# Optimization experiments

Hardware: AMD Instinct MI355X
Metric: run time of the kernel (lower is better)

The kernel has to match this reference:

```python
import jax, jax.numpy as jnp
import numpy as np

N_HEADS = 32
N_KV = 8
HEAD_DIM = 64
DIM = 2048
B, T = 4, 1024


def apply_rope(x, cos, sin):
    # x: [B, H, T, D]; cos/sin: [T, D//2]
    Tlen = x.shape[2]
    c = cos[:Tlen][None, None]  # [1,1,T,D/2]
    s = sin[:Tlen][None, None]
    x_even = x[..., 0::2]
    x_odd = x[..., 1::2]
    r_even = x_even * c - x_odd * s
    r_odd = x_even * s + x_odd * c
    # interleave back: out[...,0::2]=r_even, out[...,1::2]=r_odd
    return jnp.stack([r_even, r_odd], axis=-1).reshape(x.shape)


def setup_inputs() -> dict:
    key = jax.random.key(0)
    ks = jax.random.split(key, 7)
    sc = 0.02
    return {
        "x": jax.random.normal(ks[0], (B, T, DIM), jnp.float32),
        "cos": jax.random.normal(ks[1], (T, HEAD_DIM // 2), jnp.float32),
        "sin": jax.random.normal(ks[2], (T, HEAD_DIM // 2), jnp.float32),
        "Wq": jax.random.normal(ks[3], (N_HEADS * HEAD_DIM, DIM), jnp.float32) * sc,
        "Wk": jax.random.normal(ks[4], (N_KV * HEAD_DIM, DIM), jnp.float32) * sc,
        "Wv": jax.random.normal(ks[5], (N_KV * HEAD_DIM, DIM), jnp.float32) * sc,
        "Wo": jax.random.normal(ks[6], (DIM, N_HEADS * HEAD_DIM), jnp.float32) * sc,
    }


def reference(x, cos, sin, Wq, Wk, Wv, Wo):
    Bb, Tt, _ = x.shape
    rep = N_HEADS // N_KV
    # projections (torch Linear: y = x @ W.T)
    q = (x @ Wq.T).reshape(Bb, Tt, N_HEADS, HEAD_DIM).transpose(0, 2, 1, 3)
    k = (x @ Wk.T).reshape(Bb, Tt, N_KV, HEAD_DIM).transpose(0, 2, 1, 3)
    v = (x @ Wv.T).reshape(Bb, Tt, N_KV, HEAD_DIM).transpose(0, 2, 1, 3)
    q = apply_rope(q, cos, sin)
    k = apply_rope(k, cos, sin)
    k = jnp.repeat(k, rep, axis=1)  # [B, n_heads, T, D]
    v = jnp.repeat(v, rep, axis=1)
    scale = HEAD_DIM ** (-0.5)
    scores = jnp.einsum('bhqd,bhkd->bhqk', q, k) * scale
    causal = jnp.triu(jnp.ones((Tt, Tt), dtype=bool), k=1)
    scores = jnp.where(causal[None, None], -jnp.inf, scores)
    attn = jax.nn.softmax(scores, axis=-1)
    out = jnp.einsum('bhqk,bhkd->bhqd', attn, v)
    out = out.transpose(0, 2, 1, 3).reshape(Bb, Tt, N_HEADS * HEAD_DIM)
    return out @ Wo.T
```

## Files before the change

kernel.cpp:

```cpp
#include <hip/hip_runtime.h>
#include <math.h>

#define GAS __attribute__((address_space(1)))
#define LAS __attribute__((address_space(3)))

typedef __attribute__((ext_vector_type(4))) float f32x4;
typedef __attribute__((ext_vector_type(8))) short bf16x8;

#define MFMA(a,b,c) __builtin_amdgcn_mfma_f32_16x16x32_bf16((a),(b),(c),0,0,0)

__device__ __forceinline__ void gl_lds16(const void* g, void* l) {
    __builtin_amdgcn_global_load_lds((const GAS unsigned*)g, (LAS unsigned*)l, 16, 0, 0);
}

__device__ __forceinline__ short f2bf(float f) {
    union { float f; unsigned u; } v; v.f = f;
    unsigned r = (v.u + 0x7fff + ((v.u >> 16) & 1)) >> 16;
    return (short)r;
}

__device__ __forceinline__ void castN(const float* __restrict__ s, short* __restrict__ d,
                                      int n4, int gid, int gsz) {
    for (int i = gid; i < n4; i += gsz) {
        float4 v = ((const float4*)s)[i];
        short4 o = make_short4(f2bf(v.x), f2bf(v.y), f2bf(v.z), f2bf(v.w));
        ((short4*)d)[i] = o;
    }
}

__global__ __launch_bounds__(256)
void cast_all(const float* __restrict__ x,  const float* __restrict__ wq,
              const float* __restrict__ wk, const float* __restrict__ wv,
              const float* __restrict__ wo,
              short* __restrict__ xb, short* __restrict__ wqkv, short* __restrict__ wob) {
    int gid = blockIdx.x*256 + threadIdx.x;
    int gsz = gridDim.x*256;
    castN(x,  xb,               (4096*2048)/4, gid, gsz);
    castN(wq, wqkv,             (2048*2048)/4, gid, gsz);
    castN(wk, wqkv + 2048*2048, (512*2048)/4,  gid, gsz);
    castN(wv, wqkv + 2560*2048, (512*2048)/4,  gid, gsz);
    castN(wo, wob,              (2048*2048)/4, gid, gsz);
}

template<int MODE>
__global__ __launch_bounds__(256)
void gemm_mfma(const short* __restrict__ A, const short* __restrict__ Bw,
               int M, int N, int K, float* __restrict__ Cf,
               short* __restrict__ qo, short* __restrict__ ko, short* __restrict__ vo,
               const float* __restrict__ cosb, const float* __restrict__ sinb)
{
    __shared__ short As[128*32];
    __shared__ short Bs[128*32];
    const int tid = threadIdx.x;
    const int lane = tid & 63, wv = tid >> 6;
    const int wm = wv >> 1, wn = wv & 1;
    const int m0 = blockIdx.y*128, n0 = blockIdx.x*128;
    const int l15 = lane & 15, quad = lane >> 4;

    f32x4 acc[4][4] = {};

    const int srow = lane >> 2, skc = (lane & 3)*8;
    const short* gA0 = A  + (size_t)(m0 + wv*32 + srow)*K + skc;
    const short* gB0 = Bw + (size_t)(n0 + wv*32 + srow)*K + skc;
    short* lA = As + wv*1024;
    short* lB = Bs + wv*1024;

    for (int k0 = 0; k0 < K; k0 += 32) {
        __syncthreads();
        gl_lds16(gA0 + k0,        lA);
        gl_lds16(gA0 + 16*K + k0, lA + 512);
        gl_lds16(gB0 + k0,        lB);
        gl_lds16(gB0 + 16*K + k0, lB + 512);
        __syncthreads();
        bf16x8 af[4], bfr[4];
        #pragma unroll
        for (int t = 0; t < 4; t++) {
            af[t]  = *(const bf16x8*)&As[(wm*64 + t*16 + l15)*32 + quad*8];
            bfr[t] = *(const bf16x8*)&Bs[(wn*64 + t*16 + l15)*32 + quad*8];
        }
        #pragma unroll
        for (int i = 0; i < 4; i++)
            #pragma unroll
            for (int j = 0; j < 4; j++)
                acc[i][j] = MFMA(af[i], bfr[j], acc[i][j]);
    }

    if (MODE == 0) {
        #pragma unroll
        for (int i = 0; i < 4; i++)
            #pragma unroll
            for (int j = 0; j < 4; j++) {
                int n  = n0 + wn*64 + j*16 + l15;
                int mb = m0 + wm*64 + i*16 + quad*4;
                #pragma unroll
                for (int r = 0; r < 4; r++)
                    Cf[(size_t)(mb + r)*N + n] = acc[i][j][r];
            }
    } else {
        #pragma unroll
        for (int i = 0; i < 4; i++)
            #pragma unroll
            for (int j = 0; j < 4; j++) {
                int n  = n0 + wn*64 + j*16 + l15;
                int mb = m0 + wm*64 + i*16 + quad*4;
                if (n >= 2560) {
                    int bq = mb >> 10, t0 = mb & 1023;
                    int hv = (n - 2560) >> 6, d = (n - 2560) & 63;
                    short4 s4 = make_short4(f2bf(acc[i][j][0]), f2bf(acc[i][j][1]),
                                            f2bf(acc[i][j][2]), f2bf(acc[i][j][3]));
                    *(short4*)&vo[(((size_t)(bq*8 + hv)*64 + d) << 10) + t0] = s4;
                } else {
                    #pragma unroll
                    for (int r = 0; r < 4; r++) {
                        int m = mb + r;
                        int b = m >> 10, t = m & 1023;
                        float val = acc[i][j][r];
                        float part = __shfl_xor(val, 1);
                        int d2 = (n & 63) >> 1;
                        float c = cosb[t*32 + d2], s = sinb[t*32 + d2];
                        val = (n & 1) ? (part*s + val*c) : (val*c - part*s);
                        if (n < 2048) {
                            val *= 0.18033688f;
                            qo[(((size_t)(b*32 + (n>>6))*1024 + t) << 6) + (n & 63)] = f2bf(val);
                        } else {
                            ko[(((size_t)(b*8 + ((n-2048)>>6))*1024 + t) << 6) + ((n-2048) & 63)] = f2bf(val);
                        }
                    }
                }
            }
    }
}

__device__ __forceinline__ void stage_k(const short* __restrict__ base, short* dst,
                                        int wv, int lane) {
    #pragma unroll
    for (int jj = 0; jj < 2; jj++) {
        int j = wv*2 + jj;
        int kc = j >> 2, kr = (j & 3)*16 + (lane >> 2), dc = (lane & 3)*8;
        gl_lds16(base + (size_t)kr*64 + kc*32 + dc, dst + j*512);
    }
}

__global__ __launch_bounds__(256)
void attn_mfma(const short* __restrict__ q_ws, const short* __restrict__ k_ws,
               const short* __restrict__ vt_ws, short* __restrict__ o_ws)
{
    __shared__ short Qs[4096];
    __shared__ short Ks[2][4096];
    __shared__ short Vs[64*72];
    __shared__ short Ps[4][16*76];

    const int tid = threadIdx.x, lane = tid & 63, wv = tid >> 6;
    const int qt = 15 - blockIdx.x;
    const int h = blockIdx.y, b = blockIdx.z;
    const size_t qbase  = ((size_t)(b*32 + h))     << 16;
    const size_t kvbase = ((size_t)(b*8 + (h>>2))) << 16;
    const int l15 = lane & 15, quad = lane >> 4;
    const int nc = qt + 1;
    const int vrow = tid >> 3, vcol = (tid & 7)*8;

    #pragma unroll
    for (int jj = 0; jj < 2; jj++) {
        int j = wv*2 + jj;
        int kc = j >> 2, qr = (j & 3)*16 + (lane >> 2), dc = (lane & 3)*8;
        gl_lds16(&q_ws[qbase + (size_t)(qt*64 + qr)*64 + kc*32 + dc], &Qs[j*512]);
    }
    stage_k(k_ws + kvbase, Ks[0], wv, lane);

    f32x4 o_acc[4] = {};
    float lsum[4] = {};
    bf16x8 aq0, aq1;

    for (int c = 0; c < nc; c++) {
        const int buf = c & 1;
        __syncthreads();
        if (c == 0) {
            aq0 = *(const bf16x8*)&Qs[(wv*16 + l15)*32 + quad*8];
            aq1 = *(const bf16x8*)&Qs[2048 + (wv*16 + l15)*32 + quad*8];
        }
        const short* vp = vt_ws + kvbase + (size_t)vrow*1024 + c*64 + vcol;
        bf16x8 va = *(const bf16x8*)vp;
        bf16x8 vb = *(const bf16x8*)(vp + 32768);

        f32x4 s_acc[4];
        #pragma unroll
        for (int nt = 0; nt < 4; nt++) {
            bf16x8 bk0 = *(const bf16x8*)&Ks[buf][(nt*16 + l15)*32 + quad*8];
            bf16x8 bk1 = *(const bf16x8*)&Ks[buf][2048 + (nt*16 + l15)*32 + quad*8];
            f32x4 z = {};
            z = MFMA(aq0, bk0, z);
            s_acc[nt] = MFMA(aq1, bk1, z);
        }

        const int qrow = qt*64 + wv*16 + quad*4;
        #pragma unroll
        for (int nt = 0; nt < 4; nt++) {
            int key = c*64 + nt*16 + l15;
            #pragma unroll
            for (int r = 0; r < 4; r++) {
                float p = (key > qrow + r) ? 0.f : exp2f(s_acc[nt][r]);
                lsum[r] += p;
                Ps[wv][(quad*4 + r)*76 + nt*16 + l15] = f2bf(p);
            }
        }

        *(bf16x8*)&Vs[vrow*72 + vcol] = va;
        *(bf16x8*)&Vs[(vrow + 32)*72 + vcol] = vb;

        __syncthreads();
        if (c + 1 < nc)
            stage_k(k_ws + kvbase + (size_t)(c+1)*4096, Ks[buf^1], wv, lane);

        bf16x8 ap0 = *(const bf16x8*)&Ps[wv][l15*76 + quad*8];
        bf16x8 ap1 = *(const bf16x8*)&Ps[wv][l15*76 + 32 + quad*8];
        #pragma unroll
        for (int nt = 0; nt < 4; nt++) {
            bf16x8 bv0 = *(const bf16x8*)&Vs[(nt*16 + l15)*72 + quad*8];
            bf16x8 bv1 = *(const bf16x8*)&Vs[(nt*16 + l15)*72 + 32 + quad*8];
            o_acc[nt] = MFMA(ap0, bv0, o_acc[nt]);
            o_acc[nt] = MFMA(ap1, bv1, o_acc[nt]);
        }
    }

    #pragma unroll
    for (int r = 0; r < 4; r++) {
        lsum[r] += __shfl_xor(lsum[r], 1);
        lsum[r] += __shfl_xor(lsum[r], 2);
        lsum[r] += __shfl_xor(lsum[r], 4);
        lsum[r] += __shfl_xor(lsum[r], 8);
        float inv = 1.f / lsum[r];
        int t = qt*64 + wv*16 + quad*4 + r;
        size_t base = ((size_t)(b*1024 + t))*2048 + h*64;
        #pragma unroll
        for (int nt = 0; nt < 4; nt++)
            o_ws[base + nt*16 + l15] = f2bf(o_acc[nt][r]*inv);
    }
}

extern "C" void kernel_launch(void* const* d_in, const int* in_sizes, int n_in,
                              void* d_out, int out_size, void* d_ws, size_t ws_size,
                              hipStream_t stream) {
    const float* x    = (const float*)d_in[0];
    const float* cosb = (const float*)d_in[1];
    const float* sinb = (const float*)d_in[2];
    const float* Wq   = (const float*)d_in[3];
    const float* Wk   = (const float*)d_in[4];
    const float* Wv   = (const float*)d_in[5];
    const float* Wo   = (const float*)d_in[6];
    float* out = (float*)d_out;

    short* xb   = (short*)d_ws;
    short* wqkv = xb   + 8388608;
    short* wob  = wqkv + 6291456;
    short* q_ws = wob  + 4194304;
    short* k_ws = q_ws + 8388608;
    short* v_ws = k_ws + 2097152;
    short* o_ws = v_ws + 2097152;

    cast_all<<<2048, 256, 0, stream>>>(x, Wq, Wk, Wv, Wo, xb, wqkv, wob);
    gemm_mfma<1><<<dim3(24, 32), 256, 0, stream>>>(xb, wqkv, 4096, 3072, 2048,
                                                   nullptr, q_ws, k_ws, v_ws, cosb, sinb);
    attn_mfma<<<dim3(16, 32, 4), 256, 0, stream>>>(q_ws, k_ws, v_ws, o_ws);
    gemm_mfma<0><<<dim3(16, 32), 256, 0, stream>>>(o_ws, wob, 4096, 2048, 2048,
                                                   out, nullptr, nullptr, nullptr, nullptr, nullptr);
}
```

Measured before the change: 320.6 us.

## Compute transposed S so P stays in registers; drop Q/V/P LDS staging

The attention kernel now computes S^T (K as the A operand, Q as B), so each lane's score outputs already form the B-operand layout of a 16x16x16 bf16 MFMA for P·V. P therefore stays in registers and never goes through LDS. V fragments are loaded straight from global memory per lane, and Q is loaded directly into registers. This removes the Q/V/P shared buffers and one __syncthreads per chunk, and the next K stage is issued at the top of the loop. In exchange it uses narrower 8-byte uncoalesced V loads from global and twice as many MFMA instructions, each with half the K depth.

```diff
diff --git a/kernel.cpp b/kernel.cpp
--- a/kernel.cpp
+++ b/kernel.cpp
@@ -6,8 +6,10 @@
 
 typedef __attribute__((ext_vector_type(4))) float f32x4;
 typedef __attribute__((ext_vector_type(8))) short bf16x8;
-
-#define MFMA(a,b,c) __builtin_amdgcn_mfma_f32_16x16x32_bf16((a),(b),(c),0,0,0)
+typedef __attribute__((ext_vector_type(4))) short bf16x4;
+
+#define MFMA(a,b,c)   __builtin_amdgcn_mfma_f32_16x16x32_bf16((a),(b),(c),0,0,0)
+#define MFMA16(a,b,c) __builtin_amdgcn_mfma_f32_16x16x16bf16_1k((a),(b),(c),0,0,0)
 
 __device__ __forceinline__ void gl_lds16(const void* g, void* l) {
     __builtin_amdgcn_global_load_lds((const GAS unsigned*)g, (LAS unsigned*)l, 16, 0, 0);
@@ -145,10 +147,7 @@
 void attn_mfma(const short* __restrict__ q_ws, const short* __restrict__ k_ws,
                const short* __restrict__ vt_ws, short* __restrict__ o_ws)
 {
-    __shared__ short Qs[4096];
     __shared__ short Ks[2][4096];
-    __shared__ short Vs[64*72];
-    __shared__ short Ps[4][16*76];
 
     const int tid = threadIdx.x, lane = tid & 63, wv = tid >> 6;
     const int qt = 15 - blockIdx.x;
@@ -157,83 +156,69 @@
     const size_t kvbase = ((size_t)(b*8 + (h>>2))) << 16;
     const int l15 = lane & 15, quad = lane >> 4;
     const int nc = qt + 1;
-    const int vrow = tid >> 3, vcol = (tid & 7)*8;
-
-    #pragma unroll
-    for (int jj = 0; jj < 2; jj++) {
-        int j = wv*2 + jj;
-        int kc = j >> 2, qr = (j & 3)*16 + (lane >> 2), dc = (lane & 3)*8;
-        gl_lds16(&q_ws[qbase + (size_t)(qt*64 + qr)*64 + kc*32 + dc], &Qs[j*512]);
-    }
+
     stage_k(k_ws + kvbase, Ks[0], wv, lane);
 
+    const short* qp = q_ws + qbase + (size_t)(qt*64 + wv*16 + l15)*64 + quad*8;
+    bf16x8 aq0 = *(const bf16x8*)qp;
+    bf16x8 aq1 = *(const bf16x8*)(qp + 32);
+
     f32x4 o_acc[4] = {};
-    float lsum[4] = {};
-    bf16x8 aq0, aq1;
+    float lsum = 0.f;
+    const int qg = qt*64 + wv*16 + l15;
 
     for (int c = 0; c < nc; c++) {
         const int buf = c & 1;
         __syncthreads();
-        if (c == 0) {
-            aq0 = *(const bf16x8*)&Qs[(wv*16 + l15)*32 + quad*8];
-            aq1 = *(const bf16x8*)&Qs[2048 + (wv*16 + l15)*32 + quad*8];
+        if (c + 1 < nc)
+            stage_k(k_ws + kvbase + (size_t)(c+1)*4096, Ks[buf^1], wv, lane);
+
+        bf16x4 vf[4][4];
+        const short* vp = vt_ws + kvbase + (size_t)l15*1024 + c*64 + quad*4;
+        #pragma unroll
+        for (int dt = 0; dt < 4; dt++)
+            #pragma unroll
+            for (int nt = 0; nt < 4; nt++)
+                vf[dt][nt] = *(const bf16x4*)(vp + dt*16384 + nt*16);
+
+        f32x4 s_acc[4];
+        #pragma unroll
+        for (int nt = 0; nt < 4; nt++) {
+            bf16x8 kf0 = *(const bf16x8*)&Ks[buf][(nt*16 + l15)*32 + quad*8];
+            bf16x8 kf1 = *(const bf16x8*)&Ks[buf][2048 + (nt*16 + l15)*32 + quad*8];
+            f32x4 z = {};
+            z = MFMA(kf0, aq0, z);
+            s_acc[nt] = MFMA(kf1, aq1, z);
         }
-        const short* vp = vt_ws + kvbase + (size_t)vrow*1024 + c*64 + vcol;
-        bf16x8 va = *(const bf16x8*)vp;
-        bf16x8 vb = *(const bf16x8*)(vp + 32768);
-
-        f32x4 s_acc[4];
+
+        bf16x4 pb[4];
         #pragma unroll
         for (int nt = 0; nt < 4; nt++) {
-            bf16x8 bk0 = *(const bf16x8*)&Ks[buf][(nt*16 + l15)*32 + quad*8];
-            bf16x8 bk1 = *(const bf16x8*)&Ks[buf][2048 + (nt*16 + l15)*32 + quad*8];
-            f32x4 z = {};
-            z = MFMA(aq0, bk0, z);
-            s_acc[nt] = MFMA(aq1, bk1, z);
-        }
-
-        const int qrow = qt*64 + wv*16 + quad*4;
-        #pragma unroll
-        for (int nt = 0; nt < 4; nt++) {
-            int key = c*64 + nt*16 + l15;
+            int key0 = c*64 + nt*16 + quad*4;
             #pragma unroll
             for (int r = 0; r < 4; r++) {
-                float p = (key > qrow + r) ? 0.f : exp2f(s_acc[nt][r]);
-                lsum[r] += p;
-                Ps[wv][(quad*4 + r)*76 + nt*16 + l15] = f2bf(p);
+                float p = (key0 + r > qg) ? 0.f : exp2f(s_acc[nt][r]);
+                lsum += p;
+                pb[nt][r] = f2bf(p);
             }
         }
 
-        *(bf16x8*)&Vs[vrow*72 + vcol] = va;
-        *(bf16x8*)&Vs[(vrow + 32)*72 + vcol] = vb;
-
-        __syncthreads();
-        if (c + 1 < nc)
-            stage_k(k_ws + kvbase + (size_t)(c+1)*4096, Ks[buf^1], wv, lane);
-
-        bf16x8 ap0 = *(const bf16x8*)&Ps[wv][l15*76 + quad*8];
-        bf16x8 ap1 = *(const bf16x8*)&Ps[wv][l15*76 + 32 + quad*8];
-        #pragma unroll
-        for (int nt = 0; nt < 4; nt++) {
-            bf16x8 bv0 = *(const bf16x8*)&Vs[(nt*16 + l15)*72 + quad*8];
-            bf16x8 bv1 = *(const bf16x8*)&Vs[(nt*16 + l15)*72 + 32 + quad*8];
-            o_acc[nt] = MFMA(ap0, bv0, o_acc[nt]);
-            o_acc[nt] = MFMA(ap1, bv1, o_acc[nt]);
-        }
-    }
-
+        #pragma unroll
+        for (int dt = 0; dt < 4; dt++)
+            #pragma unroll
+            for (int nt = 0; nt < 4; nt++)
+                o_acc[dt] = MFMA16(vf[dt][nt], pb[nt], o_acc[dt]);
+    }
+
+    lsum += __shfl_xor(lsum, 16);
+    lsum += __shfl_xor(lsum, 32);
+    float inv = 1.f / lsum;
+    short* orow = o_ws + ((size_t)(b*1024 + qg))*2048 + h*64;
     #pragma unroll
-    for (int r = 0; r < 4; r++) {
-        lsum[r] += __shfl_xor(lsum[r], 1);
-        lsum[r] += __shfl_xor(lsum[r], 2);
-        lsum[r] += __shfl_xor(lsum[r], 4);
-        lsum[r] += __shfl_xor(lsum[r], 8);
-        float inv = 1.f / lsum[r];
-        int t = qt*64 + wv*16 + quad*4 + r;
-        size_t base = ((size_t)(b*1024 + t))*2048 + h*64;
-        #pragma unroll
-        for (int nt = 0; nt < 4; nt++)
-            o_ws[base + nt*16 + l15] = f2bf(o_acc[nt][r]*inv);
+    for (int dt = 0; dt < 4; dt++) {
+        short4 s4 = make_short4(f2bf(o_acc[dt][0]*inv), f2bf(o_acc[dt][1]*inv),
+                                f2bf(o_acc[dt][2]*inv), f2bf(o_acc[dt][3]*inv));
+        *(short4*)&orow[dt*16 + quad*4] = s4;
     }
 }
 
```

New measurement: 473.3 us. 1.48x slower.
